# Kernel optimization log

Measured on AMD Instinct MI355X. Metric: run time of the kernel, lower is better.

## Reference

```python
import math
import jax, jax.numpy as jnp
import numpy as np

NUM_EXPERTS = 8
TOP_K = 2
CAPACITY_FACTOR = 1.0
B, S, H, I = 4, 2048, 1024, 4096


def setup_inputs() -> dict:
    key = jax.random.key(0)
    k_x, k_rw, k_wi, k_wo = jax.random.split(key, 4)
    x = jax.random.normal(k_x, (B, S, H), dtype=jnp.float32)
    # router: nn.Linear(H, E), xavier_uniform weight, zero-ish bias
    lim = math.sqrt(6.0 / (H + NUM_EXPERTS))
    router_w = jax.random.uniform(k_rw, (NUM_EXPERTS, H), minval=-lim, maxval=lim, dtype=jnp.float32)
    router_b = jnp.zeros((NUM_EXPERTS,), dtype=jnp.float32)
    # expert weights (scaled randn for numerical sanity)
    experts_inter = jax.random.normal(k_wi, (NUM_EXPERTS - 1, H, I), dtype=jnp.float32) / math.sqrt(H)
    experts_out = jax.random.normal(k_wo, (NUM_EXPERTS - 1, I, H), dtype=jnp.float32) / math.sqrt(I)
    return {"x": x, "router_w": router_w, "router_b": router_b,
            "experts_inter": experts_inter, "experts_out": experts_out}


def reference(x, router_w, router_b, experts_inter, experts_out):
    batch, seq, hidden = x.shape
    n_exp = router_w.shape[0]
    n_tok = batch * seq
    cap = math.ceil(n_tok / n_exp * CAPACITY_FACTOR)  # expert capacity

    # router: linear + softmax
    logits = jnp.einsum('bsh,eh->bse', x, router_w) + router_b
    weights_flat = jax.nn.softmax(logits, axis=-1).reshape(n_tok, n_exp)
    x_flat = x.reshape(n_tok, hidden)

    # top-k gating; scatter topk values back into a dense [N, E] matrix
    topk_vals, topk_idx = jax.lax.top_k(weights_flat, TOP_K)
    rows = jnp.arange(n_tok)[:, None]
    topk_flat = jnp.zeros_like(weights_flat).at[rows, topk_idx].set(topk_vals)
    routing_mask = (topk_flat > 0).astype(jnp.int32)

    # no-op path = last expert column (identity * gate weight)
    noop_w = topk_flat[:, -1]
    noop_mask = routing_mask[:, -1].astype(x.dtype)

    # real experts: columns 0..E-2; capacity-limited dispatch via per-column sort
    expert_w = topk_flat[:, :-1]           # [N, E-1]
    expert_mask = routing_mask[:, :-1]     # [N, E-1]
    sorted_indices = jnp.argsort(-expert_mask, axis=0)[:cap]          # [cap, E-1]
    sorted_mask = jnp.take_along_axis(expert_mask, sorted_indices, axis=0)
    used_idx = (sorted_indices * sorted_mask).reshape(-1)             # masked -> index 0

    inputs = x_flat[used_idx] * sorted_mask.reshape(-1).astype(x.dtype)[:, None]
    inputs = inputs.reshape(cap, n_exp - 1, hidden)                   # [cap, E-1, H]
    in_w = jnp.take_along_axis(expert_w, sorted_indices, axis=0)      # [cap, E-1]

    # batched per-expert FFN
    h = jax.nn.relu(jnp.einsum('ceh,ehi->cei', inputs, experts_inter))
    out = jnp.einsum('cei,eih->ceh', h, experts_out) * in_w[..., None]

    # scatter-combine (masked slots write zeros into row 0, harmless)
    combined = jnp.zeros_like(x_flat).at[used_idx].add(out.reshape(-1, hidden))
    combined = combined + x_flat * (noop_w * noop_mask)[:, None]
    return combined.reshape(batch, seq, hidden)
```

## Files before the change

kernel.cpp:

```cpp
#include <hip/hip_runtime.h>
#include <hip/hip_bf16.h>
#include <stdint.h>
#include <stddef.h>


#define N_TOK   8192
#define HDIM    1024
#define IDIM    4096
#define NEXP    7
#define CAP     1024

typedef __bf16 bf16_t;
typedef bf16_t bf16x8 __attribute__((ext_vector_type(8)));
typedef float  f32x4  __attribute__((ext_vector_type(4)));

typedef __attribute__((address_space(3))) char lds_char_t;
typedef __attribute__((address_space(1))) const char glob_char_t;

__device__ __forceinline__ void load_lds16(const void* g, void* l) {
    __builtin_amdgcn_global_load_lds((glob_char_t*)(uintptr_t)g,
                                     (lds_char_t*)(uintptr_t)l, 16, 0, 0);
}

__device__ __forceinline__ bf16x8 pack8(const float* v) {
    bf16x8 r;
#pragma unroll
    for (int j = 0; j < 8; j++) r[j] = (bf16_t)v[j];
    return r;
}

__global__ __launch_bounds__(256) void router_kernel(
    const float* __restrict__ x, const float* __restrict__ rw,
    const float* __restrict__ rb, float* __restrict__ routew,
    float* __restrict__ out)
{
    const int wave = threadIdx.x >> 6, lane = threadIdx.x & 63;
    const int t = blockIdx.x * 4 + wave;
    const float4* xr = (const float4*)(x + (size_t)t * HDIM);
    float4 xv[4];
#pragma unroll
    for (int r = 0; r < 4; r++) xv[r] = xr[lane + r * 64];
    float p[8];
#pragma unroll
    for (int e = 0; e < 8; e++) {
        const float4* wr = (const float4*)(rw + (size_t)e * HDIM);
        float s = 0.f;
#pragma unroll
        for (int r = 0; r < 4; r++) {
            float4 wv = wr[lane + r * 64];
            s += xv[r].x * wv.x + xv[r].y * wv.y + xv[r].z * wv.z + xv[r].w * wv.w;
        }
#pragma unroll
        for (int o = 32; o; o >>= 1) s += __shfl_xor(s, o, 64);
        p[e] = s + rb[e];
    }
    float m = p[0];
#pragma unroll
    for (int e = 1; e < 8; e++) m = fmaxf(m, p[e]);
    float sum = 0.f;
#pragma unroll
    for (int e = 0; e < 8; e++) { p[e] = expf(p[e] - m); sum += p[e]; }
    float inv = 1.f / sum;
#pragma unroll
    for (int e = 0; e < 8; e++) p[e] *= inv;
    int i1 = 0;
#pragma unroll
    for (int e = 1; e < 8; e++) if (p[e] > p[i1]) i1 = e;
    int i2 = (i1 == 0) ? 1 : 0;
#pragma unroll
    for (int e = 0; e < 8; e++) if (e != i1 && p[e] > p[i2]) i2 = e;
    if (lane == 0) {
#pragma unroll
        for (int c = 0; c < 8; c++)
            routew[(size_t)t * 8 + c] = (c == i1) ? p[i1] : ((c == i2) ? p[i2] : 0.f);
    }
    const float c7 = (i1 == 7 || i2 == 7) ? p[7] : 0.f;
    float4* o = (float4*)(out + (size_t)t * HDIM);
#pragma unroll
    for (int r = 0; r < 4; r++) {
        float4 v = xv[r];
        v.x *= c7; v.y *= c7; v.z *= c7; v.w *= c7;
        o[lane + r * 64] = v;
    }
}

__global__ __launch_bounds__(1024) void compact_kernel(
    const float* __restrict__ routew, int* __restrict__ list,
    float* __restrict__ wsel)
{
    const int e = blockIdx.x;
    const int tid = threadIdx.x, wave = tid >> 6, lane = tid & 63;
    for (int i = tid; i < CAP; i += 1024) { list[e * CAP + i] = -1; wsel[e * CAP + i] = 0.f; }
    __shared__ int cnt[16];
    __syncthreads();
    int base = 0;
    const unsigned long long below = (lane == 63) ? ~0ull >> 1 : ((1ull << lane) - 1);
    for (int chunk = 0; chunk < N_TOK / 1024; chunk++) {
        const int t = chunk * 1024 + tid;
        const float w = routew[(size_t)t * 8 + e];
        const bool sel = (w > 0.f);
        const unsigned long long mask = __ballot(sel);
        const int rnk = __popcll(mask & below);
        if (lane == 0) cnt[wave] = __popcll(mask);
        __syncthreads();
        int pre = base;
        for (int w2 = 0; w2 < wave; w2++) pre += cnt[w2];
        const int rank = pre + rnk;
        if (sel && rank < CAP) { list[e * CAP + rank] = t; wsel[e * CAP + rank] = w; }
        int tot = 0;
        for (int w2 = 0; w2 < 16; w2++) tot += cnt[w2];
        base += tot;
        __syncthreads();
    }
}

__global__ __launch_bounds__(128) void gather_kernel(
    const float* __restrict__ x, const int* __restrict__ list,
    bf16_t* __restrict__ A)
{
    const int row = blockIdx.x;
    const int t = list[row];
    const int i = threadIdx.x;
    float4 v0 = {0.f, 0.f, 0.f, 0.f}, v1 = v0;
    if (t >= 0) {
        const float4* xs = (const float4*)(x + (size_t)t * HDIM);
        v0 = xs[i * 2];
        v1 = xs[i * 2 + 1];
    }
    bf16x8 o;
    o[0] = (bf16_t)v0.x; o[1] = (bf16_t)v0.y; o[2] = (bf16_t)v0.z; o[3] = (bf16_t)v0.w;
    o[4] = (bf16_t)v1.x; o[5] = (bf16_t)v1.y; o[6] = (bf16_t)v1.z; o[7] = (bf16_t)v1.w;
    ((bf16x8*)(A + (size_t)row * HDIM))[i] = o;
}

template<int K, int N>
__global__ __launch_bounds__(256) void transpose_cvt(
    const float* __restrict__ W, bf16_t* __restrict__ Wt)
{
    __shared__ float Ts[64][65];
    const int t = threadIdx.x;
    const int e = blockIdx.z;
    const int ktile = blockIdx.y * 64, ntile = blockIdx.x * 64;
    const float* We = W + (size_t)e * K * N;
    const int kr = t >> 4, nc = (t & 15) * 4;
#pragma unroll
    for (int j = 0; j < 4; j++) {
        const float4 v = *(const float4*)(We + (size_t)(ktile + kr + j * 16) * N + ntile + nc);
        Ts[nc + 0][kr + j * 16] = v.x;
        Ts[nc + 1][kr + j * 16] = v.y;
        Ts[nc + 2][kr + j * 16] = v.z;
        Ts[nc + 3][kr + j * 16] = v.w;
    }
    __syncthreads();
    const int n = t >> 2, kc = (t & 3) * 16;
    bf16_t* o = Wt + ((size_t)e * N + ntile + n) * K + ktile + kc;
    bf16x8 p0, p1;
#pragma unroll
    for (int i = 0; i < 8; i++) {
        p0[i] = (bf16_t)Ts[n][kc + i];
        p1[i] = (bf16_t)Ts[n][kc + 8 + i];
    }
    ((bf16x8*)o)[0] = p0;
    ((bf16x8*)o)[1] = p1;
}

template<int KDIM, int NDIM, int KSPLIT, bool IS_G1>
__global__ __launch_bounds__(256) void ffn_gemm_t(
    const bf16_t* __restrict__ Ab, const bf16_t* __restrict__ Bt,
    bf16_t* __restrict__ Hout, const int* __restrict__ list,
    const float* __restrict__ wsel, float* __restrict__ out)
{
    constexpr int BM = 128, BN = 128, BK = 32;
    constexpr int KLEN = KDIM / KSPLIT;
    __shared__ __align__(16) bf16_t As[2][BM * BK];
    __shared__ __align__(16) bf16_t Bs[2][BN * BK];
    const int tid = threadIdx.x, wave = tid >> 6, lane = tid & 63;
    const int e = blockIdx.z / KSPLIT, ks = blockIdx.z % KSPLIT;
    const int mblk = blockIdx.y * BM, nblk = blockIdx.x * BN;

    const bf16_t* Ae = Ab + ((size_t)e * CAP + mblk) * KDIM + (size_t)ks * KLEN;
    const bf16_t* Be = Bt + ((size_t)e * NDIM + nblk) * KDIM + (size_t)ks * KLEN;

    const int r = tid >> 2;
    const int cc = tid & 3;
    const int c = cc ^ ((r >> 1) & 3);
    const bf16_t* ag0 = Ae + (size_t)r * KDIM + c * 8;
    const bf16_t* ag1 = ag0 + (size_t)64 * KDIM;
    const bf16_t* bg0 = Be + (size_t)r * KDIM + c * 8;
    const bf16_t* bg1 = bg0 + (size_t)64 * KDIM;
    const int woff = wave * 512;

    const int wm = (wave & 1) * 64, wn = (wave >> 1) * 64;
    const int lr = lane & 15, q = lane >> 4;
    const int sw = (q ^ ((lr >> 1) & 3)) * 8;

    f32x4 acc[4][4] = {};

    load_lds16(ag0, &As[0][woff]);
    load_lds16(ag1, &As[0][2048 + woff]);
    load_lds16(bg0, &Bs[0][woff]);
    load_lds16(bg1, &Bs[0][2048 + woff]);

    int p = 0;
    for (int k0 = 0; k0 < KLEN; k0 += BK, p ^= 1) {
        const bool more = (k0 + BK < KLEN);
        if (more) {
            const int kn = k0 + BK;
            load_lds16(ag0 + kn, &As[p ^ 1][woff]);
            load_lds16(ag1 + kn, &As[p ^ 1][2048 + woff]);
            load_lds16(bg0 + kn, &Bs[p ^ 1][woff]);
            load_lds16(bg1 + kn, &Bs[p ^ 1][2048 + woff]);
            asm volatile("s_waitcnt vmcnt(4)" ::: "memory");
        } else {
            asm volatile("s_waitcnt vmcnt(0)" ::: "memory");
        }
        asm volatile("s_barrier" ::: "memory");
        bf16x8 af[4], bfr[4];
#pragma unroll
        for (int i = 0; i < 4; i++)
            af[i] = *(const bf16x8*)(&As[p][(wm + i * 16 + lr) * BK + sw]);
#pragma unroll
        for (int j = 0; j < 4; j++)
            bfr[j] = *(const bf16x8*)(&Bs[p][(wn + j * 16 + lr) * BK + sw]);
#pragma unroll
        for (int i = 0; i < 4; i++)
#pragma unroll
            for (int j = 0; j < 4; j++)
                acc[i][j] = __builtin_amdgcn_mfma_f32_16x16x32_bf16(af[i], bfr[j], acc[i][j], 0, 0, 0);
        if (more) {
            asm volatile("s_waitcnt lgkmcnt(0)" ::: "memory");
            asm volatile("s_barrier" ::: "memory");
        }
    }

    if (IS_G1) {
        bf16_t* Ho = Hout + ((size_t)e * CAP + mblk) * NDIM + nblk;
#pragma unroll
        for (int i = 0; i < 4; i++) {
            const int r0 = wm + i * 16 + q * 4;
#pragma unroll
            for (int reg = 0; reg < 4; reg++) {
                bf16_t* row = Ho + (size_t)(r0 + reg) * NDIM;
#pragma unroll
                for (int j = 0; j < 4; j++)
                    row[wn + j * 16 + lr] = (bf16_t)fmaxf(acc[i][j][reg], 0.f);
            }
        }
    } else {
#pragma unroll
        for (int i = 0; i < 4; i++) {
            const int r0 = mblk + wm + i * 16 + q * 4;
#pragma unroll
            for (int reg = 0; reg < 4; reg++) {
                const int row = r0 + reg;
                const int tok = list[e * CAP + row];
                const float wgt = wsel[e * CAP + row];
                if (tok >= 0) {
                    float* orow = out + (size_t)tok * NDIM + nblk;
#pragma unroll
                    for (int j = 0; j < 4; j++)
                        atomicAdd(orow + wn + j * 16 + lr, acc[i][j][reg] * wgt);
                }
            }
        }
    }
}

template<int KDIM, int NDIM, bool IS_G1>
__global__ __launch_bounds__(256) void ffn_gemm_fused(
    const bf16_t* __restrict__ Ab, const float* __restrict__ Wb,
    bf16_t* __restrict__ Hout, const int* __restrict__ list,
    const float* __restrict__ wsel, float* __restrict__ out)
{
    constexpr int BM = 128, BN = 128, BK = 32;
    __shared__ __align__(16) bf16_t As[BM * BK];
    __shared__ __align__(16) bf16_t Bs[BN * BK];
    const int tid = threadIdx.x, wave = tid >> 6, lane = tid & 63;
    const int e = blockIdx.z, mblk = blockIdx.y * BM, nblk = blockIdx.x * BN;

    const bf16_t* Ae = Ab + ((size_t)e * CAP + mblk) * KDIM;
    const float*  We = Wb + (size_t)e * KDIM * NDIM + nblk;

    const int ar = tid >> 2, ac = (tid & 3) * 8;
    const bf16_t* ag0 = Ae + (size_t)ar * KDIM + ac;
    const bf16_t* ag1 = ag0 + (size_t)64 * KDIM;
    bf16_t* as0 = As + wave * 512;
    bf16_t* as1 = As + 2048 + wave * 512;

    const int bn = tid & 127, bc = (tid >> 7) * 2;
    const float* bg = We + bn;
    bf16_t* bsw0 = Bs + bn * BK + ((bc ^ (bn & 3)) * 8);
    bf16_t* bsw1 = Bs + bn * BK + (((bc + 1) ^ (bn & 3)) * 8);

    const int wm = (wave & 1) * 64, wn = (wave >> 1) * 64;
    const int lr = lane & 15, q = lane >> 4;
    const int swz = q ^ ((wn + lr) & 3);

    f32x4 acc[4][4] = {};

    for (int k0 = 0; k0 < KDIM; k0 += BK) {
        load_lds16(ag0 + k0, as0);
        load_lds16(ag1 + k0, as1);
        const float* bp = bg + (size_t)(k0 + bc * 8) * NDIM;
        float v[16];
#pragma unroll
        for (int j = 0; j < 16; j++) v[j] = bp[(size_t)j * NDIM];
        bf16x8 p0 = pack8(v), p1 = pack8(v + 8);
        *(bf16x8*)bsw0 = p0;
        *(bf16x8*)bsw1 = p1;
        __syncthreads();
        bf16x8 af[4], bfr[4];
#pragma unroll
        for (int i = 0; i < 4; i++)
            af[i] = *(const bf16x8*)(As + (wm + i * 16 + lr) * BK + q * 8);
#pragma unroll
        for (int j = 0; j < 4; j++)
            bfr[j] = *(const bf16x8*)(Bs + (wn + j * 16 + lr) * BK + swz * 8);
#pragma unroll
        for (int i = 0; i < 4; i++)
#pragma unroll
            for (int j = 0; j < 4; j++)
                acc[i][j] = __builtin_amdgcn_mfma_f32_16x16x32_bf16(af[i], bfr[j], acc[i][j], 0, 0, 0);
        __syncthreads();
    }

    if (IS_G1) {
        bf16_t* Ho = Hout + ((size_t)e * CAP + mblk) * NDIM + nblk;
#pragma unroll
        for (int i = 0; i < 4; i++) {
            const int r0 = wm + i * 16 + q * 4;
#pragma unroll
            for (int reg = 0; reg < 4; reg++) {
                bf16_t* row = Ho + (size_t)(r0 + reg) * NDIM;
#pragma unroll
                for (int j = 0; j < 4; j++)
                    row[wn + j * 16 + lr] = (bf16_t)fmaxf(acc[i][j][reg], 0.f);
            }
        }
    } else {
#pragma unroll
        for (int i = 0; i < 4; i++) {
            const int r0 = mblk + wm + i * 16 + q * 4;
#pragma unroll
            for (int reg = 0; reg < 4; reg++) {
                const int row = r0 + reg;
                const int tok = list[e * CAP + row];
                const float wgt = wsel[e * CAP + row];
                if (tok >= 0) {
                    float* orow = out + (size_t)tok * NDIM + nblk;
#pragma unroll
                    for (int j = 0; j < 4; j++)
                        atomicAdd(orow + wn + j * 16 + lr, acc[i][j][reg] * wgt);
                }
            }
        }
    }
}

extern "C" void kernel_launch(void* const* d_in, const int* in_sizes, int n_in,
                              void* d_out, int out_size, void* d_ws, size_t ws_size,
                              hipStream_t stream) {
    const float* x  = (const float*)d_in[0];
    const float* rw = (const float*)d_in[1];
    const float* rb = (const float*)d_in[2];
    const float* w1 = (const float*)d_in[3];
    const float* w2 = (const float*)d_in[4];
    float* out = (float*)d_out;

    char* ws = (char*)d_ws;
    float*  routew = (float*)(ws);
    int*    list   = (int*)(ws + 262144);
    float*  wsel   = (float*)(ws + 262144 + 28672);
    bf16_t* Abuf   = (bf16_t*)(ws + 319488);
    bf16_t* Hbuf   = (bf16_t*)(ws + 14999552);
    bf16_t* Wt     = (bf16_t*)(ws + 73719808);

    const size_t NEED = 73719808ull + 58720256ull;

    router_kernel<<<N_TOK / 4, 256, 0, stream>>>(x, rw, rb, routew, out);
    compact_kernel<<<NEXP, 1024, 0, stream>>>(routew, list, wsel);
    gather_kernel<<<NEXP * CAP, 128, 0, stream>>>(x, list, Abuf);

    if (ws_size >= NEED) {
        transpose_cvt<HDIM, IDIM><<<dim3(IDIM / 64, HDIM / 64, NEXP), 256, 0, stream>>>(w1, Wt);
        ffn_gemm_t<HDIM, IDIM, 1, true><<<dim3(IDIM / 128, CAP / 128, NEXP), 256, 0, stream>>>(
            Abuf, Wt, Hbuf, nullptr, nullptr, nullptr);
        transpose_cvt<IDIM, HDIM><<<dim3(HDIM / 64, IDIM / 64, NEXP), 256, 0, stream>>>(w2, Wt);
        ffn_gemm_t<IDIM, HDIM, 2, false><<<dim3(HDIM / 128, CAP / 128, NEXP * 2), 256, 0, stream>>>(
            Hbuf, Wt, nullptr, list, wsel, out);
    } else {
        ffn_gemm_fused<HDIM, IDIM, true><<<dim3(IDIM / 128, CAP / 128, NEXP), 256, 0, stream>>>(
            Abuf, w1, Hbuf, nullptr, nullptr, nullptr);
        ffn_gemm_fused<IDIM, HDIM, false><<<dim3(HDIM / 128, CAP / 128, NEXP), 256, 0, stream>>>(
            Hbuf, w2, nullptr, list, wsel, out);
    }
}
```

Baseline: 492.8 us.

## Enlarge GEMM M-tile to 256 and use triple-buffered LDS pipeline

The expert FFN GEMM tile grows from 128x128 to 256x128, so each wave computes a 128x64 sub-tile (8x4 MFMA accumulators). Double buffering becomes a three-stage LDS ring with two tiles prefetched and explicit vmcnt waits, and launch bounds request two blocks per CU. The second GEMM's split-K rises from 2 to 4 to keep the grid large enough after halving the M-blocks. The aim is more reuse per LDS load and better latency hiding, at the cost of higher register pressure, more LDS per block and more atomic adds in the combine.

Result: slower. 531.2 us (+7.8%).

```diff
diff --git a/kernel.cpp b/kernel.cpp
--- a/kernel.cpp
+++ b/kernel.cpp
@@ -165,15 +165,16 @@
 }
 
 template<int KDIM, int NDIM, int KSPLIT, bool IS_G1>
-__global__ __launch_bounds__(256) void ffn_gemm_t(
+__global__ __launch_bounds__(256, 2) void ffn_gemm_t(
     const bf16_t* __restrict__ Ab, const bf16_t* __restrict__ Bt,
     bf16_t* __restrict__ Hout, const int* __restrict__ list,
     const float* __restrict__ wsel, float* __restrict__ out)
 {
-    constexpr int BM = 128, BN = 128, BK = 32;
+    constexpr int BM = 256, BN = 128, BK = 32;
     constexpr int KLEN = KDIM / KSPLIT;
-    __shared__ __align__(16) bf16_t As[2][BM * BK];
-    __shared__ __align__(16) bf16_t Bs[2][BN * BK];
+    constexpr int NT = KLEN / BK;
+    constexpr int STG = 8192 + 4096;
+    __shared__ __align__(16) bf16_t smem[3 * STG];
     const int tid = threadIdx.x, wave = tid >> 6, lane = tid & 63;
     const int e = blockIdx.z / KSPLIT, ks = blockIdx.z % KSPLIT;
     const int mblk = blockIdx.y * BM, nblk = blockIdx.x * BN;
@@ -184,59 +185,69 @@
     const int r = tid >> 2;
     const int cc = tid & 3;
     const int c = cc ^ ((r >> 1) & 3);
-    const bf16_t* ag0 = Ae + (size_t)r * KDIM + c * 8;
-    const bf16_t* ag1 = ag0 + (size_t)64 * KDIM;
-    const bf16_t* bg0 = Be + (size_t)r * KDIM + c * 8;
-    const bf16_t* bg1 = bg0 + (size_t)64 * KDIM;
-    const int woff = wave * 512;
-
-    const int wm = (wave & 1) * 64, wn = (wave >> 1) * 64;
+    const bf16_t* agA = Ae + (size_t)r * KDIM + c * 8;
+    const bf16_t* agB = Be + (size_t)r * KDIM + c * 8;
+    const int wbase = wave * 512;
+
+    auto stage = [&](int koff, int s) {
+        bf16_t* Ad = smem + s * STG + wbase;
+        bf16_t* Bd = smem + s * STG + 8192 + wbase;
+#pragma unroll
+        for (int j = 0; j < 4; j++)
+            load_lds16(agA + (size_t)(j * 64) * KDIM + koff, Ad + j * 2048);
+#pragma unroll
+        for (int j = 0; j < 2; j++)
+            load_lds16(agB + (size_t)(j * 64) * KDIM + koff, Bd + j * 2048);
+    };
+
+    const int wm = (wave & 1) * 128, wn = (wave >> 1) * 64;
     const int lr = lane & 15, q = lane >> 4;
     const int sw = (q ^ ((lr >> 1) & 3)) * 8;
 
-    f32x4 acc[4][4] = {};
-
-    load_lds16(ag0, &As[0][woff]);
-    load_lds16(ag1, &As[0][2048 + woff]);
-    load_lds16(bg0, &Bs[0][woff]);
-    load_lds16(bg1, &Bs[0][2048 + woff]);
-
-    int p = 0;
-    for (int k0 = 0; k0 < KLEN; k0 += BK, p ^= 1) {
-        const bool more = (k0 + BK < KLEN);
-        if (more) {
-            const int kn = k0 + BK;
-            load_lds16(ag0 + kn, &As[p ^ 1][woff]);
-            load_lds16(ag1 + kn, &As[p ^ 1][2048 + woff]);
-            load_lds16(bg0 + kn, &Bs[p ^ 1][woff]);
-            load_lds16(bg1 + kn, &Bs[p ^ 1][2048 + woff]);
-            asm volatile("s_waitcnt vmcnt(4)" ::: "memory");
+    f32x4 acc[8][4] = {};
+
+    stage(0, 0);
+    stage(BK, 1);
+
+    int pb = 0;
+    for (int kt = 0; kt < NT; kt++) {
+        if (kt + 2 < NT) {
+            int nb = pb + 2; if (nb >= 3) nb -= 3;
+            stage((kt + 2) * BK, nb);
+            asm volatile("s_waitcnt vmcnt(12)" ::: "memory");
+        } else if (kt + 2 == NT) {
+            asm volatile("s_waitcnt vmcnt(6)" ::: "memory");
         } else {
             asm volatile("s_waitcnt vmcnt(0)" ::: "memory");
         }
         asm volatile("s_barrier" ::: "memory");
-        bf16x8 af[4], bfr[4];
-#pragma unroll
-        for (int i = 0; i < 4; i++)
-            af[i] = *(const bf16x8*)(&As[p][(wm + i * 16 + lr) * BK + sw]);
+
+        const bf16_t* Ap = smem + pb * STG;
+        const bf16_t* Bp = smem + pb * STG + 8192;
+        bf16x8 af[8], bfr[4];
+#pragma unroll
+        for (int i = 0; i < 8; i++)
+            af[i] = *(const bf16x8*)(Ap + (wm + i * 16 + lr) * BK + sw);
 #pragma unroll
         for (int j = 0; j < 4; j++)
-            bfr[j] = *(const bf16x8*)(&Bs[p][(wn + j * 16 + lr) * BK + sw]);
-#pragma unroll
-        for (int i = 0; i < 4; i++)
+            bfr[j] = *(const bf16x8*)(Bp + (wn + j * 16 + lr) * BK + sw);
+#pragma unroll
+        for (int i = 0; i < 8; i++)
 #pragma unroll
             for (int j = 0; j < 4; j++)
                 acc[i][j] = __builtin_amdgcn_mfma_f32_16x16x32_bf16(af[i], bfr[j], acc[i][j], 0, 0, 0);
-        if (more) {
+
+        if (kt + 1 < NT) {
             asm volatile("s_waitcnt lgkmcnt(0)" ::: "memory");
             asm volatile("s_barrier" ::: "memory");
         }
+        pb = (pb == 2) ? 0 : pb + 1;
     }
 
     if (IS_G1) {
         bf16_t* Ho = Hout + ((size_t)e * CAP + mblk) * NDIM + nblk;
 #pragma unroll
-        for (int i = 0; i < 4; i++) {
+        for (int i = 0; i < 8; i++) {
             const int r0 = wm + i * 16 + q * 4;
 #pragma unroll
             for (int reg = 0; reg < 4; reg++) {
@@ -248,7 +259,7 @@
         }
     } else {
 #pragma unroll
-        for (int i = 0; i < 4; i++) {
+        for (int i = 0; i < 8; i++) {
             const int r0 = mblk + wm + i * 16 + q * 4;
 #pragma unroll
             for (int reg = 0; reg < 4; reg++) {
@@ -383,10 +394,10 @@
 
     if (ws_size >= NEED) {
         transpose_cvt<HDIM, IDIM><<<dim3(IDIM / 64, HDIM / 64, NEXP), 256, 0, stream>>>(w1, Wt);
-        ffn_gemm_t<HDIM, IDIM, 1, true><<<dim3(IDIM / 128, CAP / 128, NEXP), 256, 0, stream>>>(
+        ffn_gemm_t<HDIM, IDIM, 1, true><<<dim3(IDIM / 128, CAP / 256, NEXP), 256, 0, stream>>>(
             Abuf, Wt, Hbuf, nullptr, nullptr, nullptr);
         transpose_cvt<IDIM, HDIM><<<dim3(HDIM / 64, IDIM / 64, NEXP), 256, 0, stream>>>(w2, Wt);
-        ffn_gemm_t<IDIM, HDIM, 2, false><<<dim3(HDIM / 128, CAP / 128, NEXP * 2), 256, 0, stream>>>(
+        ffn_gemm_t<IDIM, HDIM, 4, false><<<dim3(HDIM / 128, CAP / 256, NEXP * 4), 256, 0, stream>>>(
             Hbuf, Wt, nullptr, list, wsel, out);
     } else {
         ffn_gemm_fused<HDIM, IDIM, true><<<dim3(IDIM / 128, CAP / 128, NEXP), 256, 0, stream>>>(
```
